# Performance work log

Measured on AMD Instinct MI355X. Metric: run time of the kernel, lower is better.

The kernel has to match this reference:

```python
import jax, jax.numpy as jnp
import numpy as np

GRID = 256

def _build_edges(g):
    ii, jj = np.meshgrid(np.arange(g), np.arange(g), indexing='ij')
    center = ii * g + jj
    srcs, tgts, attrs = [], [], []
    for di in (-1, 0, 1):
        for dj in (-1, 0, 1):
            if di == 0 and dj == 0:
                continue
            ni, nj = ii + di, jj + dj
            m = (ni >= 0) & (ni < g) & (nj >= 0) & (nj < g)
            srcs.append(center[m])
            tgts.append((ni * g + nj)[m])
            n = int(m.sum())
            a = np.empty((n, 3), np.float32)
            a[:, 0] = np.sqrt(di * di + dj * dj)
            a[:, 1] = di
            a[:, 2] = dj
            attrs.append(a)
    return (np.concatenate(srcs).astype(np.int32),
            np.concatenate(tgts).astype(np.int32),
            np.concatenate(attrs, axis=0))

def setup_inputs() -> dict:
    key = jax.random.key(0)
    ks = jax.random.split(key, 16)
    B, T, C, g = 2, 5, 10, GRID
    width, kw, out_c, Hh = 64, 32, 10, 32
    src, tgt, attr = _build_edges(g)
    nrm = lambda k, s: 0.1 * jax.random.normal(k, s, dtype=jnp.float32)
    return {
        'x': nrm(ks[0], (B, T, C, g, g)),
        'edge_src': jnp.asarray(src),
        'edge_tgt': jnp.asarray(tgt),
        'edge_attr': jnp.asarray(attr),
        'Wih0': nrm(ks[1], (4 * Hh, C)),
        'Whh0': nrm(ks[2], (4 * Hh, Hh)),
        'bih0': nrm(ks[3], (4 * Hh,)),
        'bhh0': nrm(ks[4], (4 * Hh,)),
        'Wih1': nrm(ks[5], (4 * Hh, Hh)),
        'Whh1': nrm(ks[6], (4 * Hh, Hh)),
        'bih1': nrm(ks[7], (4 * Hh,)),
        'bhh1': nrm(ks[8], (4 * Hh,)),
        'fc1_w': nrm(ks[9], (width, Hh)),
        'fc1_b': nrm(ks[10], (width,)),
        'conv_w': nrm(ks[11], (4, width, width)),
        'conv_b': nrm(ks[12], (4, width)),
        'gparam': jnp.ones((4,), jnp.float32),
        'fc2_w': nrm(ks[13], (kw, width)),
        'fc2_b': nrm(ks[14], (kw,)),
        'fc3_w': nrm(ks[15], (out_c, kw)),
        'fc3_b': jnp.zeros((out_c,), jnp.float32),
    }

def _lstm_cell(xt, h, c, Wih, Whh, bih, bhh):
    z = xt @ Wih.T + bih + h @ Whh.T + bhh
    i, f, g, o = jnp.split(z, 4, axis=-1)  # torch gate order i,f,g,o
    c = jax.nn.sigmoid(f) * c + jax.nn.sigmoid(i) * jnp.tanh(g)
    h = jax.nn.sigmoid(o) * jnp.tanh(c)
    return h, c

def _forward(x, edge_src, edge_tgt, edge_attr, Wih0, Whh0, bih0, bhh0,
             Wih1, Whh1, bih1, bhh1, fc1_w, fc1_b, conv_w, conv_b, gparam,
             fc2_w, fc2_b, fc3_w, fc3_b):
    B, T, C, H, W = x.shape
    N = H * W
    Hh = Whh0.shape[1]
    # (B,T,C,H,W) -> (T, B*N, C) sequence for the temporal LSTM over every node
    seq = x.transpose(0, 3, 4, 1, 2).reshape(B * N, T, C).transpose(1, 0, 2)

    def step(carry, xt):
        h0, c0, h1, c1 = carry
        h0, c0 = _lstm_cell(xt, h0, c0, Wih0, Whh0, bih0, bhh0)
        h1, c1 = _lstm_cell(h0, h1, c1, Wih1, Whh1, bih1, bhh1)
        return (h0, c0, h1, c1), None

    z = jnp.zeros((B * N, Hh), x.dtype)
    (h0, c0, h1, c1), _ = jax.lax.scan(step, (z, z, z, z), seq)
    feats = jax.nn.relu(h1 @ fc1_w.T + fc1_b).reshape(B, N, -1)  # (B,N,width)

    dist2 = edge_attr[:, 0:1] ** 2  # (E,1)
    depth = conv_w.shape[0]
    for k in range(depth):
        gw = jnp.exp(-dist2 / (gparam[k] ** 2 + 1e-8))       # (E,1) gaussian gate
        msg = (feats[:, edge_src] @ conv_w[k]) * gw          # (B,E,width)
        agg = jnp.zeros_like(feats).at[:, edge_tgt].add(msg) # scatter-add per batch
        feats = agg + feats @ conv_w[k] + conv_b[k]
        if k != depth - 1:
            feats = jax.nn.relu(feats)

    out = jax.nn.relu(feats @ fc2_w.T + fc2_b) @ fc3_w.T + fc3_b  # (B,N,out_c)
    out = out.reshape(B, H, W, -1).transpose(0, 3, 1, 2)[:, None]  # (B,1,out_c,H,W)
    return out

def reference(x, edge_src, edge_tgt, edge_attr, Wih0, Whh0, bih0, bhh0,
              Wih1, Whh1, bih1, bhh1, fc1_w, fc1_b, conv_w, conv_b, gparam,
              fc2_w, fc2_b, fc3_w, fc3_b):
    return _forward(x, edge_src, edge_tgt, edge_attr, Wih0, Whh0, bih0, bhh0,
                    Wih1, Whh1, bih1, bhh1, fc1_w, fc1_b, conv_w, conv_b, gparam,
                    fc2_w, fc2_b, fc3_w, fc3_b)
```

## Files before the change

kernel.cpp:

```cpp
#include <hip/hip_runtime.h>
#include <hip/hip_bf16.h>

#define NPIX   65536
#define TT     5
#define CC     10
#define HH     32
#define WIDTH  64
#define KW     32
#define OUTC   10

#define OFF_L0I    0
#define OFF_L0H    1280
#define OFF_L1I    5376
#define OFF_L1H    9472
#define OFF_B0     13568
#define OFF_B1     13696
#define OFF_FC1W   13824
#define OFF_FC1B   15872
#define OFF_CWT2   16384
#define OFF_CB     32768
#define OFF_FC2W2  33024
#define OFF_FC2B   35072
#define OFF_FC3W4  35104
#define OFF_FC3B   35424
#define OFF_GW     35440
#define OFF_FEATS_A 36864
#define OFF_FEATS_B (36864 + 8388608)

#define STRAIGHT_ATTR_IDX (65025 * 3)

__device__ __forceinline__ float sigf(float x)  { return 1.0f / (1.0f + __expf(-x)); }
__device__ __forceinline__ float tanhf_(float x){ return 1.0f - 2.0f / (__expf(2.0f * x) + 1.0f); }

__global__ __launch_bounds__(256, 1)
void prep_kernel(const float* Wih0, const float* Whh0,
                 const float* bih0, const float* bhh0,
                 const float* Wih1, const float* Whh1,
                 const float* bih1, const float* bhh1,
                 const float* fc1w, const float* fc1b,
                 const float* convw, const float* convb,
                 const float* fc2w, const float* fc2b,
                 const float* fc3w, const float* fc3b,
                 const float* gparam, const float* eattr,
                 float* P) {
    int tid = blockIdx.x * blockDim.x + threadIdx.x;
    int stride = gridDim.x * blockDim.x;
    for (int idx = tid; idx < 1280; idx += stride) {
        int g = idx & 3, j = (idx >> 2) & 31, c = idx >> 7;
        P[OFF_L0I + idx] = Wih0[(g * 32 + j) * 10 + c];
    }
    for (int idx = tid; idx < 4096; idx += stride) {
        int g = idx & 3, j = (idx >> 2) & 31, k = idx >> 7;
        P[OFF_L0H + idx] = Whh0[(g * 32 + j) * 32 + k];
        P[OFF_L1I + idx] = Wih1[(g * 32 + j) * 32 + k];
        P[OFF_L1H + idx] = Whh1[(g * 32 + j) * 32 + k];
    }
    for (int idx = tid; idx < 128; idx += stride) {
        int g = idx & 3, j = idx >> 2;
        P[OFF_B0 + idx] = bih0[g * 32 + j] + bhh0[g * 32 + j];
        P[OFF_B1 + idx] = bih1[g * 32 + j] + bhh1[g * 32 + j];
    }
    for (int idx = tid; idx < 2048; idx += stride) {
        int ch = idx & 63, k = idx >> 6;
        P[OFF_FC1W + idx] = fc1w[ch * 32 + k];
    }
    for (int i = tid; i < 64; i += stride) P[OFF_FC1B + i] = fc1b[i];
    for (int idx = tid; idx < 16384; idx += stride) {
        int k = idx >> 12, r = idx & 4095, e = r >> 1, h = r & 1;
        int co2 = e >> 6, ci = e & 63;
        P[OFF_CWT2 + idx] = convw[k * 4096 + ci * 64 + (2 * co2 + h)];
    }
    for (int i = tid; i < 256; i += stride) P[OFF_CB + i] = convb[i];
    for (int idx = tid; idx < 2048; idx += stride) {
        int e = idx >> 1, h = idx & 1, m2 = e >> 6, ch = e & 63;
        P[OFF_FC2W2 + idx] = fc2w[(2 * m2 + h) * 64 + ch];
    }
    for (int i = tid; i < 32;  i += stride) P[OFF_FC2B + i] = fc2b[i];
    for (int idx = tid; idx < 320; idx += stride) {
        int q = idx & 3, e = idx >> 2, oc2 = e >> 4, m2 = e & 15;
        int oc = 2 * oc2 + (q & 1), m = 2 * m2 + (q >> 1);
        P[OFF_FC3W4 + idx] = fc3w[oc * 32 + m];
    }
    for (int i = tid; i < 10; i += stride) P[OFF_FC3B + i] = fc3b[i];
    for (int idx = tid; idx < 8; idx += stride) {
        int k = idx >> 1;
        float g = gparam[k];
        float denom = g * g + 1e-8f;
        float a = (idx & 1) ? eattr[0] : eattr[STRAIGHT_ATTR_IDX];
        P[OFF_GW + idx] = __expf(-(a * a) / denom);
    }
}

__global__ __launch_bounds__(128, 1)
void lstm_fc1_kernel(const float* __restrict__ x,
                     const float* __restrict__ P,
                     float* __restrict__ feats) {
    __shared__ float XS[CC * 128];
    __shared__ float H0[HH * 128];
    __shared__ float H1[HH * 128];

    int tid = threadIdx.x;
    int n = blockIdx.x * 128 + tid;
    int b = n >> 16;
    int pix = n & (NPIX - 1);
    const float* xb = x + (size_t)b * TT * CC * NPIX + pix;

    float4 z[HH];
    float c0[HH], c1[HH];
#pragma unroll
    for (int j = 0; j < HH; j++) {
        c0[j] = 0.f; c1[j] = 0.f;
        H0[j * 128 + tid] = 0.f;
        H1[j * 128 + tid] = 0.f;
    }

#pragma unroll 1
    for (int t = 0; t < TT; t++) {
#pragma unroll
        for (int c = 0; c < CC; c++)
            XS[c * 128 + tid] = xb[(size_t)(t * CC + c) * NPIX];

#pragma unroll
        for (int j = 0; j < HH; j++) z[j] = *(const float4*)(P + OFF_B0 + 4 * j);
#pragma unroll 1
        for (int c = 0; c < CC; c++) {
            float xv = XS[c * 128 + tid];
            const float* wr = P + OFF_L0I + c * 128;
#pragma unroll
            for (int j = 0; j < HH; j++) {
                z[j].x = __builtin_fmaf(wr[4 * j + 0], xv, z[j].x);
                z[j].y = __builtin_fmaf(wr[4 * j + 1], xv, z[j].y);
                z[j].z = __builtin_fmaf(wr[4 * j + 2], xv, z[j].z);
                z[j].w = __builtin_fmaf(wr[4 * j + 3], xv, z[j].w);
            }
        }
#pragma unroll 1
        for (int k = 0; k < HH; k++) {
            float hv = H0[k * 128 + tid];
            const float* wr = P + OFF_L0H + k * 128;
#pragma unroll
            for (int j = 0; j < HH; j++) {
                z[j].x = __builtin_fmaf(wr[4 * j + 0], hv, z[j].x);
                z[j].y = __builtin_fmaf(wr[4 * j + 1], hv, z[j].y);
                z[j].z = __builtin_fmaf(wr[4 * j + 2], hv, z[j].z);
                z[j].w = __builtin_fmaf(wr[4 * j + 3], hv, z[j].w);
            }
        }
#pragma unroll
        for (int j = 0; j < HH; j++) {
            float cn = sigf(z[j].y) * c0[j] + sigf(z[j].x) * tanhf_(z[j].z);
            c0[j] = cn;
            H0[j * 128 + tid] = sigf(z[j].w) * tanhf_(cn);
        }

#pragma unroll
        for (int j = 0; j < HH; j++) z[j] = *(const float4*)(P + OFF_B1 + 4 * j);
#pragma unroll 1
        for (int k = 0; k < HH; k++) {
            float hv = H0[k * 128 + tid];
            const float* wr = P + OFF_L1I + k * 128;
#pragma unroll
            for (int j = 0; j < HH; j++) {
                z[j].x = __builtin_fmaf(wr[4 * j + 0], hv, z[j].x);
                z[j].y = __builtin_fmaf(wr[4 * j + 1], hv, z[j].y);
                z[j].z = __builtin_fmaf(wr[4 * j + 2], hv, z[j].z);
                z[j].w = __builtin_fmaf(wr[4 * j + 3], hv, z[j].w);
            }
        }
#pragma unroll 1
        for (int k = 0; k < HH; k++) {
            float hv = H1[k * 128 + tid];
            const float* wr = P + OFF_L1H + k * 128;
#pragma unroll
            for (int j = 0; j < HH; j++) {
                z[j].x = __builtin_fmaf(wr[4 * j + 0], hv, z[j].x);
                z[j].y = __builtin_fmaf(wr[4 * j + 1], hv, z[j].y);
                z[j].z = __builtin_fmaf(wr[4 * j + 2], hv, z[j].z);
                z[j].w = __builtin_fmaf(wr[4 * j + 3], hv, z[j].w);
            }
        }
#pragma unroll
        for (int j = 0; j < HH; j++) {
            float cn = sigf(z[j].y) * c1[j] + sigf(z[j].x) * tanhf_(z[j].z);
            c1[j] = cn;
            H1[j * 128 + tid] = sigf(z[j].w) * tanhf_(cn);
        }
    }

    float f[WIDTH];
#pragma unroll
    for (int ch = 0; ch < WIDTH; ch++) f[ch] = P[OFF_FC1B + ch];
#pragma unroll 1
    for (int k = 0; k < HH; k++) {
        float hv = H1[k * 128 + tid];
        const float* wr = P + OFF_FC1W + k * 64;
#pragma unroll
        for (int ch = 0; ch < WIDTH; ch++)
            f[ch] = __builtin_fmaf(wr[ch], hv, f[ch]);
    }
    float* fb = feats + (size_t)b * WIDTH * NPIX + pix;
#pragma unroll
    for (int ch = 0; ch < WIDTH; ch++)
        fb[(size_t)ch * NPIX] = fmaxf(f[ch], 0.f);
}

__global__ __launch_bounds__(256, 1)
void conv_fused_kernel(const float* __restrict__ Fin, float* __restrict__ Fout,
                       const float* __restrict__ P, int k) {
    __shared__ float4 CW[1024];
    __shared__ float  CB[64];
    {
        const float4* src = (const float4*)(P + OFF_CWT2 + k * 4096);
        for (int i = threadIdx.x; i < 1024; i += 256) CW[i] = src[i];
        if (threadIdx.x < 64) CB[threadIdx.x] = P[OFF_CB + k * 64 + threadIdx.x];
    }
    __syncthreads();

    int n = blockIdx.x * 256 + threadIdx.x;
    int b = n >> 16;
    int pix = n & (NPIX - 1);
    int i = pix >> 8, j = pix & 255;
    float wstr = P[OFF_GW + 2 * k], wdiag = P[OFF_GW + 2 * k + 1];
    float fu = (i > 0) ? wstr : 0.f, fd = (i < 255) ? wstr : 0.f;
    float fl = (j > 0) ? wstr : 0.f, fr = (j < 255) ? wstr : 0.f;
    float ful = (i > 0 && j > 0) ? wdiag : 0.f, fur = (i > 0 && j < 255) ? wdiag : 0.f;
    float fdl = (i < 255 && j > 0) ? wdiag : 0.f, fdr = (i < 255 && j < 255) ? wdiag : 0.f;

    const float* fb = Fin + (size_t)b * WIDTH * NPIX + pix;
    float u[WIDTH];
#pragma unroll
    for (int ch = 0; ch < WIDTH; ch++) {
        const float* yc = fb + (size_t)ch * NPIX;
        float v = yc[0];
        v += fu * yc[-256] + fd * yc[256] + fl * yc[-1] + fr * yc[1];
        v += ful * yc[-257] + fur * yc[-255] + fdl * yc[255] + fdr * yc[257];
        u[ch] = v;
    }

    float* ob = Fout + (size_t)b * WIDTH * NPIX + pix;
#pragma unroll 1
    for (int co2 = 0; co2 < 32; co2++) {
        float ax = CB[2 * co2], ay = CB[2 * co2 + 1];
        const float4* wv = CW + co2 * 32;
#pragma unroll
        for (int ci2 = 0; ci2 < 32; ci2++) {
            float4 q = wv[ci2];
            float a0 = u[2 * ci2], a1 = u[2 * ci2 + 1];
            ax = __builtin_fmaf(q.x, a0, ax); ax = __builtin_fmaf(q.z, a1, ax);
            ay = __builtin_fmaf(q.y, a0, ay); ay = __builtin_fmaf(q.w, a1, ay);
        }
        ob[(size_t)(2 * co2) * NPIX]     = fmaxf(ax, 0.f);
        ob[(size_t)(2 * co2 + 1) * NPIX] = fmaxf(ay, 0.f);
    }
}

__global__ __launch_bounds__(256, 1)
void conv_head_kernel(const float* __restrict__ Fin, const float* __restrict__ P,
                      float* __restrict__ out) {
    const int k = 3;
    __shared__ float4 CW3[1024];
    __shared__ float  CB3[64];
    __shared__ float4 F2W[512];
    __shared__ float  F2B[32];
    __shared__ float4 F3W[80];
    __shared__ float  F3B[12];
    {
        const float4* s1 = (const float4*)(P + OFF_CWT2 + k * 4096);
        for (int i = threadIdx.x; i < 1024; i += 256) CW3[i] = s1[i];
        const float4* s2 = (const float4*)(P + OFF_FC2W2);
        for (int i = threadIdx.x; i < 512; i += 256) F2W[i] = s2[i];
        const float4* s3 = (const float4*)(P + OFF_FC3W4);
        if (threadIdx.x < 80) F3W[threadIdx.x] = s3[threadIdx.x];
        if (threadIdx.x < 64) CB3[threadIdx.x] = P[OFF_CB + k * 64 + threadIdx.x];
        if (threadIdx.x < 32) F2B[threadIdx.x] = P[OFF_FC2B + threadIdx.x];
        if (threadIdx.x < 10) F3B[threadIdx.x] = P[OFF_FC3B + threadIdx.x];
    }
    __syncthreads();

    int n = blockIdx.x * 256 + threadIdx.x;
    int b = n >> 16;
    int pix = n & (NPIX - 1);
    int i = pix >> 8, j = pix & 255;
    float wstr = P[OFF_GW + 2 * k], wdiag = P[OFF_GW + 2 * k + 1];
    float fu = (i > 0) ? wstr : 0.f, fd = (i < 255) ? wstr : 0.f;
    float fl = (j > 0) ? wstr : 0.f, fr = (j < 255) ? wstr : 0.f;
    float ful = (i > 0 && j > 0) ? wdiag : 0.f, fur = (i > 0 && j < 255) ? wdiag : 0.f;
    float fdl = (i < 255 && j > 0) ? wdiag : 0.f, fdr = (i < 255 && j < 255) ? wdiag : 0.f;

    const float* fb = Fin + (size_t)b * WIDTH * NPIX + pix;
    float u[WIDTH];
#pragma unroll
    for (int ch = 0; ch < WIDTH; ch++) {
        const float* yc = fb + (size_t)ch * NPIX;
        float v = yc[0];
        v += fu * yc[-256] + fd * yc[256] + fl * yc[-1] + fr * yc[1];
        v += ful * yc[-257] + fur * yc[-255] + fdl * yc[255] + fdr * yc[257];
        u[ch] = v;
    }

    float f[WIDTH];
#pragma unroll
    for (int co2 = 0; co2 < 32; co2++) {
        float ax = CB3[2 * co2], ay = CB3[2 * co2 + 1];
        const float4* wv = CW3 + co2 * 32;
#pragma unroll
        for (int ci2 = 0; ci2 < 32; ci2++) {
            float4 q = wv[ci2];
            float a0 = u[2 * ci2], a1 = u[2 * ci2 + 1];
            ax = __builtin_fmaf(q.x, a0, ax); ax = __builtin_fmaf(q.z, a1, ax);
            ay = __builtin_fmaf(q.y, a0, ay); ay = __builtin_fmaf(q.w, a1, ay);
        }
        f[2 * co2] = ax; f[2 * co2 + 1] = ay;
    }

    float2 oo[5];
#pragma unroll
    for (int oc2 = 0; oc2 < 5; oc2++) oo[oc2] = make_float2(F3B[2 * oc2], F3B[2 * oc2 + 1]);
#pragma unroll 1
    for (int m2 = 0; m2 < 16; m2++) {
        float ax = F2B[2 * m2], ay = F2B[2 * m2 + 1];
        const float4* wv = F2W + m2 * 32;
#pragma unroll
        for (int ch2 = 0; ch2 < 32; ch2++) {
            float4 q = wv[ch2];
            ax = __builtin_fmaf(q.x, f[2 * ch2], ax); ax = __builtin_fmaf(q.z, f[2 * ch2 + 1], ax);
            ay = __builtin_fmaf(q.y, f[2 * ch2], ay); ay = __builtin_fmaf(q.w, f[2 * ch2 + 1], ay);
        }
        ax = fmaxf(ax, 0.f); ay = fmaxf(ay, 0.f);
#pragma unroll
        for (int oc2 = 0; oc2 < 5; oc2++) {
            float4 q = F3W[oc2 * 16 + m2];
            oo[oc2].x += q.x * ax + q.z * ay;
            oo[oc2].y += q.y * ax + q.w * ay;
        }
    }
    float* ob = out + (size_t)b * OUTC * NPIX + pix;
#pragma unroll
    for (int oc2 = 0; oc2 < 5; oc2++) {
        ob[(size_t)(2 * oc2) * NPIX]     = oo[oc2].x;
        ob[(size_t)(2 * oc2 + 1) * NPIX] = oo[oc2].y;
    }
}

extern "C" void kernel_launch(void* const* d_in, const int* in_sizes, int n_in,
                              void* d_out, int out_size, void* d_ws, size_t ws_size,
                              hipStream_t stream) {
    const float* x     = (const float*)d_in[0];
    const float* eattr = (const float*)d_in[3];
    const float* Wih0  = (const float*)d_in[4];
    const float* Whh0  = (const float*)d_in[5];
    const float* bih0  = (const float*)d_in[6];
    const float* bhh0  = (const float*)d_in[7];
    const float* Wih1  = (const float*)d_in[8];
    const float* Whh1  = (const float*)d_in[9];
    const float* bih1  = (const float*)d_in[10];
    const float* bhh1  = (const float*)d_in[11];
    const float* fc1w  = (const float*)d_in[12];
    const float* fc1b  = (const float*)d_in[13];
    const float* convw = (const float*)d_in[14];
    const float* convb = (const float*)d_in[15];
    const float* gparam= (const float*)d_in[16];
    const float* fc2w  = (const float*)d_in[17];
    const float* fc2b  = (const float*)d_in[18];
    const float* fc3w  = (const float*)d_in[19];
    const float* fc3b  = (const float*)d_in[20];

    float* P  = (float*)d_ws;
    float* FA = P + OFF_FEATS_A;
    float* FB = P + OFF_FEATS_B;

    prep_kernel<<<64, 256, 0, stream>>>(Wih0, Whh0, bih0, bhh0, Wih1, Whh1, bih1, bhh1,
                                        fc1w, fc1b, convw, convb, fc2w, fc2b, fc3w, fc3b,
                                        gparam, eattr, P);
    lstm_fc1_kernel<<<1024, 128, 0, stream>>>(x, P, FA);
    conv_fused_kernel<<<512, 256, 0, stream>>>(FA, FB, P, 0);
    conv_fused_kernel<<<512, 256, 0, stream>>>(FB, FA, P, 1);
    conv_fused_kernel<<<512, 256, 0, stream>>>(FA, FB, P, 2);
    conv_head_kernel<<<512, 256, 0, stream>>>(FB, P, (float*)d_out);
}
```

Before: 638.4 us.

## Keep LSTM hidden state in registers and compute gates in groups of eight units

The LSTM kernel now keeps the hidden states h0 and h1 in registers instead of shared memory, and fully unrolls the input and recurrent loops. Gate pre-activations are computed in four groups of 8 hidden units (32 accumulators each) instead of all 128 at once. The prep kernel reorders the packed weights to match this grouped access. This removes shared-memory traffic and rolled-loop overhead, but full unrolling greatly enlarges the code and raises register pressure (h0, h1, c0, c1, hn, z), which risks spills.

```diff
diff --git a/kernel.cpp b/kernel.cpp
--- a/kernel.cpp
+++ b/kernel.cpp
@@ -46,14 +46,17 @@
     int tid = blockIdx.x * blockDim.x + threadIdx.x;
     int stride = gridDim.x * blockDim.x;
     for (int idx = tid; idx < 1280; idx += stride) {
-        int g = idx & 3, j = (idx >> 2) & 31, c = idx >> 7;
-        P[OFF_L0I + idx] = Wih0[(g * 32 + j) * 10 + c];
+        int g = idx & 3, j8 = (idx >> 2) & 7, rest = idx >> 5;
+        int c = rest % 10, grp = rest / 10;
+        P[OFF_L0I + idx] = Wih0[(g * 32 + grp * 8 + j8) * 10 + c];
     }
     for (int idx = tid; idx < 4096; idx += stride) {
-        int g = idx & 3, j = (idx >> 2) & 31, k = idx >> 7;
-        P[OFF_L0H + idx] = Whh0[(g * 32 + j) * 32 + k];
-        P[OFF_L1I + idx] = Wih1[(g * 32 + j) * 32 + k];
-        P[OFF_L1H + idx] = Whh1[(g * 32 + j) * 32 + k];
+        int g = idx & 3, j8 = (idx >> 2) & 7, rest = idx >> 5;
+        int k = rest & 31, grp = rest >> 5;
+        int row = (g * 32 + grp * 8 + j8) * 32 + k;
+        P[OFF_L0H + idx] = Whh0[row];
+        P[OFF_L1I + idx] = Wih1[row];
+        P[OFF_L1H + idx] = Whh1[row];
     }
     for (int idx = tid; idx < 128; idx += stride) {
         int g = idx & 3, j = idx >> 2;
@@ -95,108 +98,92 @@
 void lstm_fc1_kernel(const float* __restrict__ x,
                      const float* __restrict__ P,
                      float* __restrict__ feats) {
-    __shared__ float XS[CC * 128];
-    __shared__ float H0[HH * 128];
-    __shared__ float H1[HH * 128];
-
     int tid = threadIdx.x;
     int n = blockIdx.x * 128 + tid;
     int b = n >> 16;
     int pix = n & (NPIX - 1);
     const float* xb = x + (size_t)b * TT * CC * NPIX + pix;
 
-    float4 z[HH];
-    float c0[HH], c1[HH];
-#pragma unroll
-    for (int j = 0; j < HH; j++) {
-        c0[j] = 0.f; c1[j] = 0.f;
-        H0[j * 128 + tid] = 0.f;
-        H1[j * 128 + tid] = 0.f;
-    }
+    float h0[HH], h1[HH], c0[HH], c1[HH], hn[HH];
+#pragma unroll
+    for (int j = 0; j < HH; j++) { h0[j] = 0.f; h1[j] = 0.f; c0[j] = 0.f; c1[j] = 0.f; }
 
 #pragma unroll 1
     for (int t = 0; t < TT; t++) {
-#pragma unroll
-        for (int c = 0; c < CC; c++)
-            XS[c * 128 + tid] = xb[(size_t)(t * CC + c) * NPIX];
-
-#pragma unroll
-        for (int j = 0; j < HH; j++) z[j] = *(const float4*)(P + OFF_B0 + 4 * j);
-#pragma unroll 1
-        for (int c = 0; c < CC; c++) {
-            float xv = XS[c * 128 + tid];
-            const float* wr = P + OFF_L0I + c * 128;
-#pragma unroll
-            for (int j = 0; j < HH; j++) {
-                z[j].x = __builtin_fmaf(wr[4 * j + 0], xv, z[j].x);
-                z[j].y = __builtin_fmaf(wr[4 * j + 1], xv, z[j].y);
-                z[j].z = __builtin_fmaf(wr[4 * j + 2], xv, z[j].z);
-                z[j].w = __builtin_fmaf(wr[4 * j + 3], xv, z[j].w);
-            }
-        }
-#pragma unroll 1
-        for (int k = 0; k < HH; k++) {
-            float hv = H0[k * 128 + tid];
-            const float* wr = P + OFF_L0H + k * 128;
-#pragma unroll
-            for (int j = 0; j < HH; j++) {
-                z[j].x = __builtin_fmaf(wr[4 * j + 0], hv, z[j].x);
-                z[j].y = __builtin_fmaf(wr[4 * j + 1], hv, z[j].y);
-                z[j].z = __builtin_fmaf(wr[4 * j + 2], hv, z[j].z);
-                z[j].w = __builtin_fmaf(wr[4 * j + 3], hv, z[j].w);
-            }
-        }
-#pragma unroll
-        for (int j = 0; j < HH; j++) {
-            float cn = sigf(z[j].y) * c0[j] + sigf(z[j].x) * tanhf_(z[j].z);
-            c0[j] = cn;
-            H0[j * 128 + tid] = sigf(z[j].w) * tanhf_(cn);
-        }
-
-#pragma unroll
-        for (int j = 0; j < HH; j++) z[j] = *(const float4*)(P + OFF_B1 + 4 * j);
-#pragma unroll 1
-        for (int k = 0; k < HH; k++) {
-            float hv = H0[k * 128 + tid];
-            const float* wr = P + OFF_L1I + k * 128;
-#pragma unroll
-            for (int j = 0; j < HH; j++) {
-                z[j].x = __builtin_fmaf(wr[4 * j + 0], hv, z[j].x);
-                z[j].y = __builtin_fmaf(wr[4 * j + 1], hv, z[j].y);
-                z[j].z = __builtin_fmaf(wr[4 * j + 2], hv, z[j].z);
-                z[j].w = __builtin_fmaf(wr[4 * j + 3], hv, z[j].w);
-            }
-        }
-#pragma unroll 1
-        for (int k = 0; k < HH; k++) {
-            float hv = H1[k * 128 + tid];
-            const float* wr = P + OFF_L1H + k * 128;
-#pragma unroll
-            for (int j = 0; j < HH; j++) {
-                z[j].x = __builtin_fmaf(wr[4 * j + 0], hv, z[j].x);
-                z[j].y = __builtin_fmaf(wr[4 * j + 1], hv, z[j].y);
-                z[j].z = __builtin_fmaf(wr[4 * j + 2], hv, z[j].z);
-                z[j].w = __builtin_fmaf(wr[4 * j + 3], hv, z[j].w);
-            }
-        }
-#pragma unroll
-        for (int j = 0; j < HH; j++) {
-            float cn = sigf(z[j].y) * c1[j] + sigf(z[j].x) * tanhf_(z[j].z);
-            c1[j] = cn;
-            H1[j * 128 + tid] = sigf(z[j].w) * tanhf_(cn);
-        }
+        float xt[CC];
+#pragma unroll
+        for (int c = 0; c < CC; c++) xt[c] = xb[(size_t)(t * CC + c) * NPIX];
+
+#pragma unroll
+        for (int grp = 0; grp < 4; grp++) {
+            float z[32];
+#pragma unroll
+            for (int e = 0; e < 32; e++) z[e] = P[OFF_B0 + grp * 32 + e];
+#pragma unroll
+            for (int c = 0; c < CC; c++) {
+                const float* wr = P + OFF_L0I + (grp * 10 + c) * 32;
+#pragma unroll
+                for (int e = 0; e < 32; e++) z[e] = __builtin_fmaf(wr[e], xt[c], z[e]);
+            }
+#pragma unroll
+            for (int k = 0; k < HH; k++) {
+                const float* wr = P + OFF_L0H + (grp * 32 + k) * 32;
+#pragma unroll
+                for (int e = 0; e < 32; e++) z[e] = __builtin_fmaf(wr[e], h0[k], z[e]);
+            }
+#pragma unroll
+            for (int j8 = 0; j8 < 8; j8++) {
+                int j = grp * 8 + j8;
+                float zi = z[j8 * 4 + 0], zf = z[j8 * 4 + 1];
+                float zg = z[j8 * 4 + 2], zo = z[j8 * 4 + 3];
+                float cn = sigf(zf) * c0[j] + sigf(zi) * tanhf_(zg);
+                c0[j] = cn;
+                hn[j] = sigf(zo) * tanhf_(cn);
+            }
+        }
+#pragma unroll
+        for (int j = 0; j < HH; j++) h0[j] = hn[j];
+
+#pragma unroll
+        for (int grp = 0; grp < 4; grp++) {
+            float z[32];
+#pragma unroll
+            for (int e = 0; e < 32; e++) z[e] = P[OFF_B1 + grp * 32 + e];
+#pragma unroll
+            for (int k = 0; k < HH; k++) {
+                const float* wr = P + OFF_L1I + (grp * 32 + k) * 32;
+#pragma unroll
+                for (int e = 0; e < 32; e++) z[e] = __builtin_fmaf(wr[e], h0[k], z[e]);
+            }
+#pragma unroll
+            for (int k = 0; k < HH; k++) {
+                const float* wr = P + OFF_L1H + (grp * 32 + k) * 32;
+#pragma unroll
+                for (int e = 0; e < 32; e++) z[e] = __builtin_fmaf(wr[e], h1[k], z[e]);
+            }
+#pragma unroll
+            for (int j8 = 0; j8 < 8; j8++) {
+                int j = grp * 8 + j8;
+                float zi = z[j8 * 4 + 0], zf = z[j8 * 4 + 1];
+                float zg = z[j8 * 4 + 2], zo = z[j8 * 4 + 3];
+                float cn = sigf(zf) * c1[j] + sigf(zi) * tanhf_(zg);
+                c1[j] = cn;
+                hn[j] = sigf(zo) * tanhf_(cn);
+            }
+        }
+#pragma unroll
+        for (int j = 0; j < HH; j++) h1[j] = hn[j];
     }
 
     float f[WIDTH];
 #pragma unroll
     for (int ch = 0; ch < WIDTH; ch++) f[ch] = P[OFF_FC1B + ch];
-#pragma unroll 1
+#pragma unroll
     for (int k = 0; k < HH; k++) {
-        float hv = H1[k * 128 + tid];
         const float* wr = P + OFF_FC1W + k * 64;
 #pragma unroll
         for (int ch = 0; ch < WIDTH; ch++)
-            f[ch] = __builtin_fmaf(wr[ch], hv, f[ch]);
+            f[ch] = __builtin_fmaf(wr[ch], h1[k], f[ch]);
     }
     float* fb = feats + (size_t)b * WIDTH * NPIX + pix;
 #pragma unroll
```

After: 1.530 ms. +139.8%, slower.
